# Kernel optimization log

Hardware: AMD Instinct MI355X
Metric: run time of the kernel (lower is better)

## Reference

```python
import jax, jax.numpy as jnp
import numpy as np
import math

IN_FEATURES = 512
KERNEL = 3
EPS = 1e-08
GAIN = 1.0 / math.sqrt(IN_FEATURES * KERNEL * KERNEL)  # lr_multiplier=1


def setup_inputs() -> dict:
    key = jax.random.key(0)
    k1, k2, k3 = jax.random.split(key, 3)
    x = jax.random.normal(k1, (16, 512, 32, 32), dtype=jnp.float32)
    style = jax.random.normal(k2, (16, 512), dtype=jnp.float32)
    weight = jax.random.normal(k3, (512, 512, 3, 3), dtype=jnp.float32)
    return {"x": x, "style": style, "weight": weight}


def reference(x, style, weight):
    # w: [B, O, I, k, k] = gain-scaled weight modulated per-sample by style over input channels
    w = (weight * GAIN)[None] * style[:, None, :, None, None]
    # demodulate: rsqrt of sum of squares over (I, kh, kw) per (B, O)
    sigma = jax.lax.rsqrt(jnp.sum(jnp.square(w), axis=(2, 3, 4)) + EPS)
    w = w * sigma[:, :, None, None, None]
    # per-sample conv2d with padding='same' (stride 1, k=3 -> pad 1)
    def conv_one(xi, wi):  # xi: [C,H,W], wi: [O,I,k,k]
        return jax.lax.conv_general_dilated(
            xi[None], wi, window_strides=(1, 1), padding='SAME',
            dimension_numbers=('NCHW', 'OIHW', 'NCHW'))[0]
    return jax.vmap(conv_one)(x, w)  # [B, O, H, W]
```

## Files before the change

### kernel.cpp

```cpp
#include <hip/hip_runtime.h>
#include <hip/hip_bf16.h>

#define EPSF 1e-8f
#define GAINF 0.014731391274719739f

typedef __attribute__((ext_vector_type(8))) __bf16 bf16x8;
typedef __attribute__((ext_vector_type(4))) __bf16 bf16x4;
typedef __attribute__((ext_vector_type(16))) float f32x16;

#define GLOAD_LDS16(gp, lp) __builtin_amdgcn_global_load_lds( \
    (const __attribute__((address_space(1))) unsigned int*)(gp), \
    (__attribute__((address_space(3))) unsigned int*)(lp), 16, 0, 0)

__global__ void k_prep(const float* __restrict__ x, const float* __restrict__ style,
                       const float* __restrict__ w,
                       __hip_bfloat16* __restrict__ wbf, __hip_bfloat16* __restrict__ xs,
                       float* __restrict__ esc) {
  int blk = blockIdx.x, tid = threadIdx.x;
  if (blk < 2048) {
    __shared__ float tile[64][65];
    int b = blk >> 7, rem = blk & 127, ct = rem >> 4, pt = rem & 15;
    int p0 = pt * 64, c0 = ct * 64;
    int tx = tid & 63, ty = tid >> 6;
#pragma unroll
    for (int k = 0; k < 16; ++k) {
      int ci = ty + k * 4;
      tile[ci][tx] = x[((b * 512) + (c0 + ci)) * 1024 + p0 + tx];
    }
    __syncthreads();
    int tq = tid & 15, py = tid >> 4;
    int c = c0 + tq * 4;
    int cb = c >> 5, cw = c & 31;
    float st0 = style[b * 512 + c], st1 = style[b * 512 + c + 1];
    float st2 = style[b * 512 + c + 2], st3 = style[b * 512 + c + 3];
#pragma unroll
    for (int k = 0; k < 4; ++k) {
      int pl = py + k * 16;
      int p = p0 + pl;
      int y = p >> 5, xx = p & 31;
      int site = (y + 1) * 34 + (xx + 1);
      bf16x4 v;
      v[0] = (__bf16)(tile[tq * 4 + 0][pl] * st0);
      v[1] = (__bf16)(tile[tq * 4 + 1][pl] * st1);
      v[2] = (__bf16)(tile[tq * 4 + 2][pl] * st2);
      v[3] = (__bf16)(tile[tq * 4 + 3][pl] * st3);
      *reinterpret_cast<bf16x4*>(xs + (size_t)(((b * 16 + cb) * 1156 + site) * 32 + cw)) = v;
    }
  } else if (blk < 2560) {
    __shared__ float red[4][16];
    int o = blk - 2048;
    float pacc[16];
#pragma unroll
    for (int b = 0; b < 16; ++b) pacc[b] = 0.f;
#pragma unroll
    for (int half = 0; half < 2; ++half) {
      int i = tid + half * 256;
      const float* p = w + (size_t)(o * 512 + i) * 9;
      float s = 0.f;
#pragma unroll
      for (int t = 0; t < 9; ++t) {
        float v = p[t];
        s += v * v;
        wbf[(size_t)t * 262144 + (i >> 5) * 16384 + o * 32 + (i & 31)] = __float2bfloat16(v);
      }
#pragma unroll
      for (int b = 0; b < 16; ++b) {
        float st = style[b * 512 + i];
        pacc[b] += st * st * s;
      }
    }
#pragma unroll
    for (int b = 0; b < 16; ++b)
#pragma unroll
      for (int off = 32; off; off >>= 1) pacc[b] += __shfl_down(pacc[b], off);
    int lane = tid & 63, wv2 = tid >> 6;
    if (lane == 0)
#pragma unroll
      for (int b = 0; b < 16; ++b) red[wv2][b] = pacc[b];
    __syncthreads();
    if (tid < 16) {
      float s = red[0][tid] + red[1][tid] + red[2][tid] + red[3][tid];
      esc[tid * 512 + o] = GAINF * rsqrtf(s * (GAINF * GAINF) + EPSF);
    }
  } else {
    int bb = blk - 2560;
    int b = bb >> 4, cb = bb & 15;
    for (int i2 = tid; i2 < 528; i2 += 256) {
      int sb = i2 >> 2, q = i2 & 3;
      int yp, xp;
      if (sb < 34) { yp = 0; xp = sb; }
      else if (sb < 68) { yp = 33; xp = sb - 34; }
      else { int t2 = sb - 68; yp = 1 + (t2 >> 1); xp = (t2 & 1) * 33; }
      float4 z = {0.f, 0.f, 0.f, 0.f};
      *reinterpret_cast<float4*>(xs + (size_t)(((b * 16 + cb) * 1156 + yp * 34 + xp) * 32 + q * 8)) = z;
    }
  }
}

__global__ __launch_bounds__(256, 2) void k_conv(
    const __hip_bfloat16* __restrict__ wbf, const __hip_bfloat16* __restrict__ xs,
    const float* __restrict__ esc, float* __restrict__ out) {
  __shared__ __hip_bfloat16 ldsB[2 * 6528];
  int g = blockIdx.x;
  int xcd = g & 7, sblk = g >> 3;
  int mg = sblk >> 4;
  int n = xcd * 16 + (sblk & 15);
  int b = n >> 3, nt = n & 7;
  int row0 = nt * 4;
  int tid = threadIdx.x;
  int wv = tid >> 6, lane = tid & 63;
  int l31 = lane & 31, lhi = lane >> 5;
  int o_base = mg * 128 + wv * 32;

  int roff[4];
#pragma unroll
  for (int j = 0; j < 4; ++j) {
    int idx = wv * 204 + j * 64 + lane;
    int site = idx >> 2, q0 = idx & 3;
    int qs = q0 ^ ((site >> 1) & 3);
    roff[j] = site * 32 + qs * 8;
  }

#define STAGE(cbv) do { \
    const __hip_bfloat16* _g = xs + (size_t)((b * 16 + (cbv)) * 1156 + row0 * 34) * 32; \
    __hip_bfloat16* _l = ldsB + ((cbv) & 1) * 6528 + wv * 1632 + lane * 8; \
    _Pragma("unroll") \
    for (int _j = 0; _j < 3; ++_j) GLOAD_LDS16(_g + roff[_j], _l + _j * 512); \
    if (lane < 12) GLOAD_LDS16(_g + roff[3], _l + 3 * 512); \
  } while (0)

  int wrow = (o_base + l31) * 32 + lhi * 8;
#define LOADA(dst, t_, cb_) do { \
    const __hip_bfloat16* _p = wbf + (size_t)(t_) * 262144 + (cb_) * 16384 + wrow; \
    dst[0] = *reinterpret_cast<const bf16x8*>(_p); \
    dst[1] = *reinterpret_cast<const bf16x8*>(_p + 16); \
  } while (0)

  f32x16 acc[4];
#pragma unroll
  for (int j = 0; j < 4; ++j)
#pragma unroll
    for (int e = 0; e < 16; ++e) acc[j][e] = 0.f;

  bf16x8 aC[2], aN[2];
  STAGE(0);
  LOADA(aC, 0, 0);

  for (int cb = 0; cb < 16; ++cb) {
    __syncthreads();
    if (cb < 15) STAGE(cb + 1);
    const __hip_bfloat16* lb = ldsB + (cb & 1) * 6528;
#pragma unroll
    for (int t = 0; t < 9; ++t) {
      const int dy = t / 3, dx = t - dy * 3;
      if (cb < 15 || t < 8) {
        int tn = (t == 8) ? 0 : t + 1;
        int cbn = (t == 8) ? cb + 1 : cb;
        LOADA(aN, tn, cbn);
      }
      int s[4], sw[4];
#pragma unroll
      for (int ns = 0; ns < 4; ++ns) {
        s[ns] = (ns + dy) * 34 + l31 + dx;
        sw[ns] = (s[ns] >> 1) & 3;
      }
#pragma unroll
      for (int k2 = 0; k2 < 2; ++k2) {
        int ko = (k2 << 1) | lhi;
        bf16x8 bf[4];
#pragma unroll
        for (int ns = 0; ns < 4; ++ns)
          bf[ns] = *reinterpret_cast<const bf16x8*>(&lb[(s[ns] * 4 + (ko ^ sw[ns])) * 8]);
#pragma unroll
        for (int ns = 0; ns < 4; ++ns)
          acc[ns] = __builtin_amdgcn_mfma_f32_32x32x16_bf16(aC[k2], bf[ns], acc[ns], 0, 0, 0);
      }
      aC[0] = aN[0];
      aC[1] = aN[1];
    }
  }
  int pxb = nt * 128 + l31;
#pragma unroll
  for (int reg = 0; reg < 16; ++reg) {
    int o = o_base + (reg & 3) + ((reg >> 2) << 3) + (lhi << 2);
    float e = esc[(b << 9) + o];
#pragma unroll
    for (int ns = 0; ns < 4; ++ns)
      out[(size_t)((b << 9) + o) * 1024 + pxb + ns * 32] = acc[ns][reg] * e;
  }
#undef STAGE
#undef LOADA
}

extern "C" void kernel_launch(void* const* d_in, const int* in_sizes, int n_in,
                              void* d_out, int out_size, void* d_ws, size_t ws_size,
                              hipStream_t stream) {
  const float* x = (const float*)d_in[0];
  const float* style = (const float*)d_in[1];
  const float* w = (const float*)d_in[2];
  float* out = (float*)d_out;
  char* ws = (char*)d_ws;
  __hip_bfloat16* wbf = (__hip_bfloat16*)(ws);
  __hip_bfloat16* xs  = (__hip_bfloat16*)(ws + 4718592);
  float* esc = (float*)(ws + 23658496);

  hipLaunchKernelGGL(k_prep, dim3(2816), dim3(256), 0, stream, x, style, w, wbf, xs, esc);
  hipLaunchKernelGGL(k_conv, dim3(512), dim3(256), 0, stream, wbf, xs, esc, out);
}
```

Measured before the change: 161.5 us.

## Use chunk-major LDS layout for activations and deepen weight prefetch to two taps

Replaces the XOR-swizzled site-major LDS layout with a chunk-major layout where each wave stages one 8-channel chunk for all 204 sites, so B-fragment reads become contiguous per chunk and the swizzle arithmetic disappears. The global loads now stride by 64 bytes per lane instead of being contiguous, which may reduce coalescing. The weight (A) fragment prefetch is extended from one tap ahead to two taps ahead with a three-register rotation, hiding more global-load latency at the cost of extra VGPRs under the 2-waves launch bound.

```diff
diff --git a/kernel.cpp b/kernel.cpp
--- a/kernel.cpp
+++ b/kernel.cpp
@@ -112,21 +112,12 @@
   int l31 = lane & 31, lhi = lane >> 5;
   int o_base = mg * 128 + wv * 32;
 
-  int roff[4];
-#pragma unroll
-  for (int j = 0; j < 4; ++j) {
-    int idx = wv * 204 + j * 64 + lane;
-    int site = idx >> 2, q0 = idx & 3;
-    int qs = q0 ^ ((site >> 1) & 3);
-    roff[j] = site * 32 + qs * 8;
-  }
-
 #define STAGE(cbv) do { \
-    const __hip_bfloat16* _g = xs + (size_t)((b * 16 + (cbv)) * 1156 + row0 * 34) * 32; \
+    const __hip_bfloat16* _g = xs + (size_t)((b * 16 + (cbv)) * 1156 + row0 * 34) * 32 + wv * 8; \
     __hip_bfloat16* _l = ldsB + ((cbv) & 1) * 6528 + wv * 1632 + lane * 8; \
     _Pragma("unroll") \
-    for (int _j = 0; _j < 3; ++_j) GLOAD_LDS16(_g + roff[_j], _l + _j * 512); \
-    if (lane < 12) GLOAD_LDS16(_g + roff[3], _l + 3 * 512); \
+    for (int _j = 0; _j < 3; ++_j) GLOAD_LDS16(_g + (_j * 64 + lane) * 32, _l + _j * 512); \
+    if (lane < 12) GLOAD_LDS16(_g + (192 + lane) * 32, _l + 3 * 512); \
   } while (0)
 
   int wrow = (o_base + l31) * 32 + lhi * 8;
@@ -142,9 +133,10 @@
 #pragma unroll
     for (int e = 0; e < 16; ++e) acc[j][e] = 0.f;
 
-  bf16x8 aC[2], aN[2];
+  bf16x8 aQ0[2], aQ1[2], aQ2[2];
   STAGE(0);
-  LOADA(aC, 0, 0);
+  LOADA(aQ0, 0, 0);
+  LOADA(aQ1, 1, 0);
 
   for (int cb = 0; cb < 16; ++cb) {
     __syncthreads();
@@ -153,30 +145,29 @@
 #pragma unroll
     for (int t = 0; t < 9; ++t) {
       const int dy = t / 3, dx = t - dy * 3;
-      if (cb < 15 || t < 8) {
-        int tn = (t == 8) ? 0 : t + 1;
-        int cbn = (t == 8) ? cb + 1 : cb;
-        LOADA(aN, tn, cbn);
-      }
-      int s[4], sw[4];
-#pragma unroll
-      for (int ns = 0; ns < 4; ++ns) {
+      {
+        const int t2 = t + 2;
+        const int tn = (t2 >= 9) ? t2 - 9 : t2;
+        int cbn = (t2 >= 9) ? cb + 1 : cb;
+        if (cbn < 16) LOADA(aQ2, tn, cbn);
+      }
+      int s[4];
+#pragma unroll
+      for (int ns = 0; ns < 4; ++ns)
         s[ns] = (ns + dy) * 34 + l31 + dx;
-        sw[ns] = (s[ns] >> 1) & 3;
-      }
 #pragma unroll
       for (int k2 = 0; k2 < 2; ++k2) {
         int ko = (k2 << 1) | lhi;
         bf16x8 bf[4];
 #pragma unroll
         for (int ns = 0; ns < 4; ++ns)
-          bf[ns] = *reinterpret_cast<const bf16x8*>(&lb[(s[ns] * 4 + (ko ^ sw[ns])) * 8]);
+          bf[ns] = *reinterpret_cast<const bf16x8*>(&lb[(ko * 204 + s[ns]) * 8]);
 #pragma unroll
         for (int ns = 0; ns < 4; ++ns)
-          acc[ns] = __builtin_amdgcn_mfma_f32_32x32x16_bf16(aC[k2], bf[ns], acc[ns], 0, 0, 0);
-      }
-      aC[0] = aN[0];
-      aC[1] = aN[1];
+          acc[ns] = __builtin_amdgcn_mfma_f32_32x32x16_bf16(aQ0[k2], bf[ns], acc[ns], 0, 0, 0);
+      }
+      aQ0[0] = aQ1[0]; aQ0[1] = aQ1[1];
+      aQ1[0] = aQ2[0]; aQ1[1] = aQ2[1];
     }
   }
   int pxb = nt * 128 + l31;
```

After: 167.0 us. 3.4% more time.
